# Kernel optimization log

Hardware: AMD Instinct MI355X
Metric: run time of the kernel (lower is better)

Reference implementation:

```python
import jax, jax.numpy as jnp
import numpy as np

B, S, H, A, I = 64, 512, 1024, 1024, 1024


def setup_inputs() -> dict:
    key = jax.random.key(0)
    ks = jax.random.split(key, 12)
    s = lambda fan_in: 1.0 / np.sqrt(fan_in)
    return {
        "encoded": jax.random.normal(ks[0], (B, S, H), jnp.float32),
        "inputs": jax.random.normal(ks[1], (B, I), jnp.float32),
        "states": jax.random.normal(ks[2], (B, H), jnp.float32),
        # attention params
        "W_enc": jax.random.uniform(ks[3], (H, A), jnp.float32, -s(H), s(H)),
        "b_enc": jnp.zeros((A,), jnp.float32),
        "W_dec": jax.random.uniform(ks[4], (H, A), jnp.float32, -s(H), s(H)),
        "b_dec": jnp.zeros((A,), jnp.float32),
        "w_out": jax.random.uniform(ks[5], (A, 1), jnp.float32, -s(A), s(A)),
        "b_out": jnp.zeros((1,), jnp.float32),
        # GRU cell params (input size = I + H)
        "W_ih": jax.random.uniform(ks[6], (3 * H, I + H), jnp.float32, -s(H), s(H)),
        "W_hh": jax.random.uniform(ks[7], (3 * H, H), jnp.float32, -s(H), s(H)),
        "b_ih": jax.random.uniform(ks[8], (3 * H,), jnp.float32, -s(H), s(H)),
        "b_hh": jax.random.uniform(ks[9], (3 * H,), jnp.float32, -s(H), s(H)),
    }


def reference(encoded, inputs, states, W_enc, b_enc, W_dec, b_dec, w_out, b_out,
              W_ih, W_hh, b_ih, b_hh):
    # setup_memory: project encoder states  [B,S,H] @ [H,A] -> [B,S,A]
    enc_proj = jnp.einsum("bsh,ha->bsa", encoded, W_enc) + b_enc
    # project decoder state and broadcast over S
    dec_proj = states @ W_dec + b_dec                      # [B,A]
    projected = enc_proj + dec_proj[:, None, :]            # [B,S,A]
    scores = jnp.tanh(projected) @ w_out + b_out           # [B,S,1]
    weights = jax.nn.softmax(scores, axis=1)               # [B,S,1]
    attention = jnp.sum(encoded * weights, axis=1)         # [B,H]
    # GRU cell on concatenated input
    x = jnp.concatenate([inputs, attention], axis=1)       # [B,I+H]
    gi = x @ W_ih.T + b_ih                                 # [B,3H]
    gh = states @ W_hh.T + b_hh                            # [B,3H]
    i_r, i_z, i_n = jnp.split(gi, 3, axis=1)
    h_r, h_z, h_n = jnp.split(gh, 3, axis=1)
    r = jax.nn.sigmoid(i_r + h_r)
    z = jax.nn.sigmoid(i_z + h_z)
    n = jnp.tanh(i_n + r * h_n)
    return (1.0 - z) * n + z * states                      # [B,H]
```

## Files before the change

kernel.cpp:

```cpp
#include <hip/hip_runtime.h>
#include <stdint.h>

typedef __bf16 bf16x8 __attribute__((ext_vector_type(8)));
typedef float f32x4 __attribute__((ext_vector_type(4)));

#define LOG2E 1.4426950408889634f
#define LSTR 32

__device__ __forceinline__ unsigned short f2bf(float f) {
  unsigned int x = __builtin_bit_cast(unsigned int, f);
  x += 0x7FFFu + ((x >> 16) & 1u);
  return (unsigned short)(x >> 16);
}
__device__ __forceinline__ float bflo(unsigned int u) {
  return __builtin_bit_cast(float, u << 16);
}
__device__ __forceinline__ float bfhi(unsigned int u) {
  return __builtin_bit_cast(float, u & 0xffff0000u);
}
__device__ __forceinline__ float tanh_fast(float x) {
  float cx = fminf(fmaxf(x, -15.f), 15.f);
  float e = __builtin_amdgcn_exp2f(cx * (2.f * LOG2E));
  return (e - 1.f) * __builtin_amdgcn_rcpf(e + 1.f);
}
__device__ __forceinline__ float sigmoid_fast(float x) {
  float cx = fminf(fmaxf(x, -30.f), 30.f);
  float e = __builtin_amdgcn_exp2f(cx * LOG2E);
  return e * __builtin_amdgcn_rcpf(e + 1.f);
}
__device__ __forceinline__ ushort4 cvt4(const float4 f) {
  return make_ushort4(f2bf(f.x), f2bf(f.y), f2bf(f.z), f2bf(f.w));
}

__device__ __forceinline__ void gl_lds16(const unsigned short* g,
                                         const unsigned short* lds_base) {
  __builtin_amdgcn_global_load_lds(
      (const __attribute__((address_space(1))) unsigned int*)(uintptr_t)g,
      (__attribute__((address_space(3))) unsigned int*)(unsigned int)(uintptr_t)lds_base,
      16, 0, 0);
}

__global__ __launch_bounds__(256) void k_prep(
    const float* __restrict__ W_enc, unsigned short* __restrict__ Wt,
    const float* __restrict__ states, const float* __restrict__ W_dec,
    const float* __restrict__ b_dec, const float* __restrict__ b_enc,
    float* __restrict__ dvec, float4* __restrict__ zbase,
    const float* __restrict__ enc, unsigned short* __restrict__ encb) {
  __shared__ unsigned short tile[64][65];
  __shared__ float red[256];
  const int bid = blockIdx.x;
  const int tid = threadIdx.x;
  if (bid < 256) {
    const int bx = bid & 15, by = bid >> 4;
    const int x = tid & 63, y0 = tid >> 6;
#pragma unroll
    for (int i = y0; i < 64; i += 4)
      tile[i][x] = f2bf(W_enc[(size_t)(by * 64 + i) * 1024 + bx * 64 + x]);
    __syncthreads();
#pragma unroll
    for (int i = y0; i < 64; i += 4)
      Wt[(size_t)(bx * 64 + i) * 1024 + by * 64 + x] = tile[x][i];
  } else if (bid < 768) {
    const int bb = bid - 256;
    const int b = bb >> 3;
    const int a0 = (bb & 7) * 128;
    const int a = tid & 127, half = tid >> 7;
    const float* sp = states + (size_t)b * 1024;
    const float* wp = W_dec + a0 + a;
    float acc = 0.f;
    const int kb = half * 512;
#pragma unroll 8
    for (int k = kb; k < kb + 512; ++k)
      acc += sp[k] * wp[(size_t)k * 1024];
    red[tid] = acc;
    __syncthreads();
    if (tid < 128) {
      float v = red[tid] + red[tid + 128];
      dvec[(size_t)b * 1024 + a0 + tid] = v + b_dec[a0 + tid] + b_enc[a0 + tid];
    }
  } else if (bid < 1248) {
    const float4 z = {0.f, 0.f, 0.f, 0.f};
    zbase[(size_t)(bid - 768) * 256 + tid] = z;
  } else {
    const size_t i = ((size_t)(bid - 1248) * 256 + tid) * 8;
    const float4 f0 = *(const float4*)(enc + i);
    const float4 f1 = *(const float4*)(enc + i + 4);
    *(ushort4*)(encb + i) = cvt4(f0);
    *(ushort4*)(encb + i + 4) = cvt4(f1);
  }
}

__global__ __launch_bounds__(256, 3) void k_scores_bf16(
    const unsigned short* __restrict__ encb,
    const unsigned short* __restrict__ Wt,
    const float* __restrict__ dvec,
    const float* __restrict__ w_out,
    float* __restrict__ scores) {
  __shared__ alignas(16) unsigned short lds[2][8192];
  __shared__ float sc[128];

  const int tid = threadIdx.x;
  const int wave = tid >> 6, lane = tid & 63;
  const int l15 = lane & 15, quad = lane >> 4;
  const int xcd = blockIdx.x & 7;
  const int kb_ = blockIdx.x >> 3;
  const int mt = ((kb_ >> 3) << 3) | xcd;
  const int nt = kb_ & 7;
  const int row0 = mt * 128;
  const int b = row0 >> 9;
  const int wm = (wave >> 1) * 64, wn = (wave & 1) * 64;
  const int srow = lane >> 2;
  const int fsw = ((lane >> 2) & 3) ^ ((lane >> 4) & 3);
  const int skoff = (((lane & 3) ^ fsw) * 8);
  const int rchunk = ((quad ^ ((l15 & 3) ^ ((l15 >> 2) & 3))) * 8);

  if (tid < 128) sc[tid] = 0.f;

  const unsigned short* gsrc[4];
#pragma unroll
  for (int s = 0; s < 4; ++s) {
    const int g = wave * 4 + s;
    gsrc[s] = (g < 8)
        ? encb + (size_t)(row0 + g * 16 + srow) * 1024 + skoff
        : Wt + (size_t)(nt * 128 + (g - 8) * 16 + srow) * 1024 + skoff;
  }

  const f32x4 vz = {0.f, 0.f, 0.f, 0.f};
  f32x4 acc[4][4];
#pragma unroll
  for (int i = 0; i < 4; ++i)
#pragma unroll
    for (int j = 0; j < 4; ++j) acc[i][j] = vz;

#define STAGE(BUF, KK)                                              \
  do {                                                              \
    _Pragma("unroll") for (int s = 0; s < 4; ++s)                   \
        gl_lds16(gsrc[s] + (KK), &lds[BUF][(wave * 4 + s) * 512]);  \
  } while (0)

#define COMPUTE(BUF)                                                          \
  do {                                                                        \
    bf16x8 af[4], bg[4];                                                      \
    _Pragma("unroll") for (int i = 0; i < 4; ++i)                             \
        af[i] = *(const bf16x8*)(&lds[BUF][(wm + i * 16 + l15) * LSTR + rchunk]); \
    _Pragma("unroll") for (int j = 0; j < 4; ++j)                             \
        bg[j] = *(const bf16x8*)(&lds[BUF][4096 + (wn + j * 16 + l15) * LSTR + rchunk]); \
    _Pragma("unroll") for (int i = 0; i < 4; ++i)                             \
      _Pragma("unroll") for (int j = 0; j < 4; ++j)                           \
          acc[i][j] = __builtin_amdgcn_mfma_f32_16x16x32_bf16(af[i], bg[j],   \
                                                              acc[i][j], 0, 0, 0); \
  } while (0)

  STAGE(0, 0);
  __syncthreads();

#pragma unroll 1
  for (int k0 = 0; k0 < 1024; k0 += 64) {
    STAGE(1, k0 + 32);
    COMPUTE(0);
    __syncthreads();
    if (k0 + 64 < 1024) { STAGE(0, k0 + 64); }
    COMPUTE(1);
    __syncthreads();
  }
#undef STAGE
#undef COMPUTE

  float p[4][4];
#pragma unroll
  for (int i = 0; i < 4; ++i)
#pragma unroll
    for (int r = 0; r < 4; ++r) p[i][r] = 0.f;
#pragma unroll
  for (int j = 0; j < 4; ++j) {
    const int a = nt * 128 + wn + j * 16 + l15;
    const float dv = dvec[(size_t)b * 1024 + a];
    const float wo = w_out[a];
#pragma unroll
    for (int i = 0; i < 4; ++i)
#pragma unroll
      for (int r = 0; r < 4; ++r)
        p[i][r] += tanh_fast(acc[i][j][r] + dv) * wo;
  }
#pragma unroll
  for (int i = 0; i < 4; ++i)
#pragma unroll
    for (int r = 0; r < 4; ++r) {
      float v = p[i][r];
      v += __shfl_xor(v, 1);
      v += __shfl_xor(v, 2);
      v += __shfl_xor(v, 4);
      v += __shfl_xor(v, 8);
      if (l15 == 0) atomicAdd(&sc[wm + i * 16 + quad * 4 + r], v);
    }
  __syncthreads();
  if (tid < 128)
    atomicAdd(&scores[(size_t)b * 512 + (row0 & 511) + tid], sc[tid]);
}

__global__ __launch_bounds__(256) void k_scores_f32(
    const float* __restrict__ enc, const unsigned short* __restrict__ Wt,
    const float* __restrict__ dvec, const float* __restrict__ w_out,
    float* __restrict__ scores) {
  __shared__ alignas(16) unsigned short lA[128 * LSTR];
  __shared__ alignas(16) unsigned short lB[128 * LSTR];
  __shared__ float sc[128];
  const int tid = threadIdx.x;
  const int wave = tid >> 6, lane = tid & 63;
  const int l15 = lane & 15, quad = lane >> 4;
  const int mt = blockIdx.x >> 2, nh = blockIdx.x & 3;
  const int row0 = mt * 128, b = row0 >> 9;
  const int wm = (wave >> 1) * 64, wn = (wave & 1) * 64;
  const int srow = lane >> 2, skoff = (lane & 3) * 8;
  if (tid < 128) sc[tid] = 0.f;
  const f32x4 vz = {0.f, 0.f, 0.f, 0.f};
#pragma unroll 1
  for (int t2 = 0; t2 < 2; ++t2) {
    const int nt = nh * 2 + t2;
    f32x4 acc[4][4];
#pragma unroll
    for (int i = 0; i < 4; ++i)
#pragma unroll
      for (int j = 0; j < 4; ++j) acc[i][j] = vz;
#pragma unroll 1
    for (int k0 = 0; k0 < 1024; k0 += 32) {
      ushort4 sa[2][2];
      uint4 vb[2];
#pragma unroll
      for (int rr = 0; rr < 2; ++rr) {
        const int r = wave * 2 + rr;
        const float* ap = enc + (size_t)(row0 + r * 16 + srow) * 1024 + k0 + skoff;
        sa[rr][0] = cvt4(*(const float4*)ap);
        sa[rr][1] = cvt4(*(const float4*)(ap + 4));
        vb[rr] = *(const uint4*)(Wt + (size_t)(nt * 128 + r * 16 + srow) * 1024 + k0 + skoff);
      }
      __syncthreads();
#pragma unroll
      for (int rr = 0; rr < 2; ++rr) {
        const int r = wave * 2 + rr;
        *(ushort4*)(lA + (r * 16 + srow) * LSTR + skoff) = sa[rr][0];
        *(ushort4*)(lA + (r * 16 + srow) * LSTR + skoff + 4) = sa[rr][1];
        *(uint4*)(lB + (r * 16 + srow) * LSTR + skoff) = vb[rr];
      }
      __syncthreads();
      bf16x8 af[4], bg[4];
#pragma unroll
      for (int i = 0; i < 4; ++i)
        af[i] = *(const bf16x8*)(lA + (wm + i * 16 + l15) * LSTR + quad * 8);
#pragma unroll
      for (int j = 0; j < 4; ++j)
        bg[j] = *(const bf16x8*)(lB + (wn + j * 16 + l15) * LSTR + quad * 8);
#pragma unroll
      for (int i = 0; i < 4; ++i)
#pragma unroll
        for (int j = 0; j < 4; ++j)
          acc[i][j] = __builtin_amdgcn_mfma_f32_16x16x32_bf16(af[i], bg[j],
                                                              acc[i][j], 0, 0, 0);
    }
    float p[4][4];
#pragma unroll
    for (int i = 0; i < 4; ++i)
#pragma unroll
      for (int r = 0; r < 4; ++r) p[i][r] = 0.f;
#pragma unroll
    for (int j = 0; j < 4; ++j) {
      const int a = nt * 128 + wn + j * 16 + l15;
      const float dv = dvec[(size_t)b * 1024 + a];
      const float wo = w_out[a];
#pragma unroll
      for (int i = 0; i < 4; ++i)
#pragma unroll
        for (int r = 0; r < 4; ++r)
          p[i][r] += tanh_fast(acc[i][j][r] + dv) * wo;
    }
#pragma unroll
    for (int i = 0; i < 4; ++i)
#pragma unroll
      for (int r = 0; r < 4; ++r) {
        float v = p[i][r];
        v += __shfl_xor(v, 1);
        v += __shfl_xor(v, 2);
        v += __shfl_xor(v, 4);
        v += __shfl_xor(v, 8);
        if (l15 == 0) atomicAdd(&sc[wm + i * 16 + quad * 4 + r], v);
      }
  }
  __syncthreads();
  if (tid < 128)
    atomicAdd(&scores[(size_t)b * 512 + (row0 & 511) + tid], sc[tid]);
}

template <bool ABF16>
__global__ __launch_bounds__(256) void k_attn(const void* __restrict__ encv,
                                              const float* __restrict__ scores,
                                              float* __restrict__ att) {
  const int b = blockIdx.x >> 2;
  const int scn = blockIdx.x & 3;
  const int tid = threadIdx.x;
  __shared__ float w[512];
  __shared__ float redm[4], reds[4];

  const float s0 = scores[(size_t)b * 512 + tid];
  const float s1 = scores[(size_t)b * 512 + 256 + tid];
  float m = fmaxf(s0, s1);
#pragma unroll
  for (int off = 32; off; off >>= 1) m = fmaxf(m, __shfl_xor(m, off));
  const int wv = tid >> 6;
  if ((tid & 63) == 0) redm[wv] = m;
  __syncthreads();
  m = fmaxf(fmaxf(redm[0], redm[1]), fmaxf(redm[2], redm[3]));
  const float e0 = __builtin_amdgcn_exp2f((s0 - m) * LOG2E);
  const float e1 = __builtin_amdgcn_exp2f((s1 - m) * LOG2E);
  float sum = e0 + e1;
#pragma unroll
  for (int off = 32; off; off >>= 1) sum += __shfl_xor(sum, off);
  if ((tid & 63) == 0) reds[wv] = sum;
  __syncthreads();
  sum = reds[0] + reds[1] + reds[2] + reds[3];
  const float inv = 1.f / sum;
  w[tid] = e0 * inv;
  w[tid + 256] = e1 * inv;
  __syncthreads();

  const int h0 = (tid & 127) * 8;
  const int sh = tid >> 7;
  float a[8];
#pragma unroll
  for (int i = 0; i < 8; ++i) a[i] = 0.f;
  const size_t base = ((size_t)(b * 512 + scn * 128 + sh)) * 1024 + h0;
#pragma unroll 4
  for (int i = 0; i < 64; ++i) {
    const float ws_ = w[scn * 128 + sh + 2 * i];
    if constexpr (ABF16) {
      const uint4 v = *(const uint4*)((const unsigned short*)encv + base + (size_t)(2 * i) * 1024);
      a[0] += ws_ * bflo(v.x); a[1] += ws_ * bfhi(v.x);
      a[2] += ws_ * bflo(v.y); a[3] += ws_ * bfhi(v.y);
      a[4] += ws_ * bflo(v.z); a[5] += ws_ * bfhi(v.z);
      a[6] += ws_ * bflo(v.w); a[7] += ws_ * bfhi(v.w);
    } else {
      const float* ep = (const float*)encv + base + (size_t)(2 * i) * 1024;
      const float4 v0 = *(const float4*)ep;
      const float4 v1 = *(const float4*)(ep + 4);
      a[0] += ws_ * v0.x; a[1] += ws_ * v0.y;
      a[2] += ws_ * v0.z; a[3] += ws_ * v0.w;
      a[4] += ws_ * v1.x; a[5] += ws_ * v1.y;
      a[6] += ws_ * v1.z; a[7] += ws_ * v1.w;
    }
  }
#pragma unroll
  for (int i = 0; i < 8; ++i)
    atomicAdd(&att[(size_t)b * 1024 + h0 + i], a[i]);
}

__global__ __launch_bounds__(256) void k_gru_gemm(
    const float* __restrict__ xin,
    const float* __restrict__ att,
    const float* __restrict__ states,
    const float* __restrict__ W_ih,
    const float* __restrict__ W_hh,
    float* __restrict__ gbuf) {
  const int tid = threadIdx.x;
  const int wave = tid >> 6, lane = tid & 63;
  const int l15 = lane & 15, quad = lane >> 4;
  const int kk = blockIdx.x & 3;
  const int rest = blockIdx.x >> 2;
  const bool is_gh = rest >= 48;
  const int nt = is_gh ? rest - 48 : rest;
  const int n0 = nt * 64;
  const int KT = is_gh ? 1024 : 2048;
  const int Kh = KT >> 2;
  const int kbase = kk * Kh;
  const float* W = is_gh ? W_hh : W_ih;
  float* outp = gbuf + (is_gh ? (size_t)64 * 3072 : 0);

  __shared__ alignas(16) unsigned short lA[64 * LSTR];
  __shared__ alignas(16) unsigned short lB[64 * LSTR];

  const f32x4 vz = {0.f, 0.f, 0.f, 0.f};
  f32x4 acc[2][2];
  acc[0][0] = vz; acc[0][1] = vz; acc[1][0] = vz; acc[1][1] = vz;

  const int arow = tid >> 2;
  const int achunk = (tid & 3) * 8;
  const int fswG = ((tid >> 2) & 3) ^ ((tid >> 4) & 3);
  const int wchunk = (((tid & 3) ^ fswG) * 8);
  const int rchunkG = ((quad ^ ((l15 & 3) ^ ((l15 >> 2) & 3))) * 8);
  const int wm2 = (wave >> 1) * 32, wn2 = (wave & 1) * 32;

  float4 ra0, ra1, rb0, rb1;
  auto LOADK = [&](int kg0) {
    const int kg = kg0 + achunk;
    const float* ap = is_gh ? (states + (size_t)arow * 1024 + kg)
                    : (kg < 1024 ? (xin + (size_t)arow * 1024 + kg)
                                 : (att + (size_t)arow * 1024 + (kg - 1024)));
    ra0 = *(const float4*)ap;
    ra1 = *(const float4*)(ap + 4);
    const float* wp = W + (size_t)(n0 + arow) * KT + kg;
    rb0 = *(const float4*)wp;
    rb1 = *(const float4*)(wp + 4);
  };
  LOADK(kbase);

#pragma unroll 1
  for (int k0 = 0; k0 < Kh; k0 += 32) {
    __syncthreads();
    *(ushort4*)(lA + arow * LSTR + wchunk) = cvt4(ra0);
    *(ushort4*)(lA + arow * LSTR + wchunk + 4) = cvt4(ra1);
    *(ushort4*)(lB + arow * LSTR + wchunk) = cvt4(rb0);
    *(ushort4*)(lB + arow * LSTR + wchunk + 4) = cvt4(rb1);
    __syncthreads();
    if (k0 + 32 < Kh) LOADK(kbase + k0 + 32);
    bf16x8 af[2], bg[2];
#pragma unroll
    for (int i = 0; i < 2; ++i)
      af[i] = *(const bf16x8*)(lA + (wm2 + i * 16 + l15) * LSTR + rchunkG);
#pragma unroll
    for (int j = 0; j < 2; ++j)
      bg[j] = *(const bf16x8*)(lB + (wn2 + j * 16 + l15) * LSTR + rchunkG);
#pragma unroll
    for (int i = 0; i < 2; ++i)
#pragma unroll
      for (int j = 0; j < 2; ++j)
        acc[i][j] = __builtin_amdgcn_mfma_f32_16x16x32_bf16(af[i], bg[j],
                                                            acc[i][j], 0, 0, 0);
  }
#pragma unroll
  for (int i = 0; i < 2; ++i)
#pragma unroll
    for (int j = 0; j < 2; ++j)
#pragma unroll
      for (int r = 0; r < 4; ++r) {
        const int m = wm2 + i * 16 + quad * 4 + r;
        const int n = n0 + wn2 + j * 16 + l15;
        atomicAdd(&outp[(size_t)m * 3072 + n], acc[i][j][r]);
      }
}

__global__ void k_gate(const float* __restrict__ gbuf,
                       const float* __restrict__ states,
                       const float* __restrict__ b_ih,
                       const float* __restrict__ b_hh,
                       float* __restrict__ outp) {
  const int idx = blockIdx.x * 256 + threadIdx.x;
  const int b = idx >> 10, h = idx & 1023;
  const float* gi = gbuf + (size_t)b * 3072;
  const float* gh = gbuf + (size_t)64 * 3072 + (size_t)b * 3072;
  const float ir = gi[h] + b_ih[h];
  const float iz = gi[1024 + h] + b_ih[1024 + h];
  const float in_ = gi[2048 + h] + b_ih[2048 + h];
  const float hr = gh[h] + b_hh[h];
  const float hz = gh[1024 + h] + b_hh[1024 + h];
  const float hn = gh[2048 + h] + b_hh[2048 + h];
  const float r = sigmoid_fast(ir + hr);
  const float z = sigmoid_fast(iz + hz);
  const float n = tanh_fast(in_ + r * hn);
  const float hp = states[idx];
  outp[idx] = (1.f - z) * n + z * hp;
}

extern "C" void kernel_launch(void* const* d_in, const int* in_sizes, int n_in,
                              void* d_out, int out_size, void* d_ws, size_t ws_size,
                              hipStream_t stream) {
  const float* enc    = (const float*)d_in[0];
  const float* xin    = (const float*)d_in[1];
  const float* states = (const float*)d_in[2];
  const float* W_enc  = (const float*)d_in[3];
  const float* b_enc  = (const float*)d_in[4];
  const float* W_dec  = (const float*)d_in[5];
  const float* b_dec  = (const float*)d_in[6];
  const float* w_out  = (const float*)d_in[7];
  const float* W_ih   = (const float*)d_in[9];
  const float* W_hh   = (const float*)d_in[10];
  const float* b_ih   = (const float*)d_in[11];
  const float* b_hh   = (const float*)d_in[12];
  float* out = (float*)d_out;

  const size_t ENC_BF16_BYTES = (size_t)32768 * 1024 * 2;
  const bool use_bf16 = ws_size >= ENC_BF16_BYTES + (8u << 20);

  char* ws = (char*)d_ws;
  unsigned short* encb = (unsigned short*)ws;
  char* base = ws + (use_bf16 ? ENC_BF16_BYTES : 0);
  unsigned short* Wt = (unsigned short*)base;
  float* dvec    = (float*)(base + 2097152);
  float* scoresb = (float*)(base + 2097152 + 262144);
  float* att     = (float*)(base + 2097152 + 262144 + 131072);
  float* gbuf    = (float*)(base + 2097152 + 262144 + 131072 + 262144);

  const int prep_grid = use_bf16 ? 17632 : 1248;
  k_prep<<<prep_grid, 256, 0, stream>>>(W_enc, Wt, states, W_dec, b_dec, b_enc,
                                        dvec, (float4*)scoresb, enc, encb);
  if (use_bf16) {
    k_scores_bf16<<<2048, 256, 0, stream>>>(encb, Wt, dvec, w_out, scoresb);
    k_attn<true><<<256, 256, 0, stream>>>(encb, scoresb, att);
  } else {
    k_scores_f32<<<1024, 256, 0, stream>>>(enc, Wt, dvec, w_out, scoresb);
    k_attn<false><<<256, 256, 0, stream>>>(enc, scoresb, att);
  }
  k_gru_gemm<<<384, 256, 0, stream>>>(xin, att, states, W_ih, W_hh, gbuf);
  k_gate<<<256, 256, 0, stream>>>(gbuf, states, b_ih, b_hh, out);
}
```

Measured before the change: 405.5 us.

## Replace atomic accumulations in attention and GRU GEMM with deterministic reductions

The attention kernel now gives each block the full sequence for a 128-wide slice of H. It reduces partial sums across sequence groups in LDS and stores the result directly, so float atomics into att are gone. The GRU GEMM writes each split-K partial to its own plane of gbuf, and the gate kernel sums the four planes. With att and gbuf no longer accumulated through atomics, the prep kernel zeroes only the scores buffer, which cuts most of the zero-fill blocks. In exchange, the gate kernel reads more memory, the attention kernel adds LDS reduction barriers, and gbuf now reuses the start of the bf16 encoder workspace after that data is consumed.

```diff
diff --git a/kernel.cpp b/kernel.cpp
--- a/kernel.cpp
+++ b/kernel.cpp
@@ -78,11 +78,11 @@
       float v = red[tid] + red[tid + 128];
       dvec[(size_t)b * 1024 + a0 + tid] = v + b_dec[a0 + tid] + b_enc[a0 + tid];
     }
-  } else if (bid < 1248) {
+  } else if (bid < 800) {
     const float4 z = {0.f, 0.f, 0.f, 0.f};
     zbase[(size_t)(bid - 768) * 256 + tid] = z;
   } else {
-    const size_t i = ((size_t)(bid - 1248) * 256 + tid) * 8;
+    const size_t i = ((size_t)(bid - 800) * 256 + tid) * 8;
     const float4 f0 = *(const float4*)(enc + i);
     const float4 f1 = *(const float4*)(enc + i + 4);
     *(ushort4*)(encb + i) = cvt4(f0);
@@ -294,11 +294,12 @@
 __global__ __launch_bounds__(256) void k_attn(const void* __restrict__ encv,
                                               const float* __restrict__ scores,
                                               float* __restrict__ att) {
-  const int b = blockIdx.x >> 2;
-  const int scn = blockIdx.x & 3;
+  const int b = blockIdx.x >> 3;
+  const int hch = blockIdx.x & 7;
   const int tid = threadIdx.x;
   __shared__ float w[512];
   __shared__ float redm[4], reds[4];
+  __shared__ float red[16][132];
 
   const float s0 = scores[(size_t)b * 512 + tid];
   const float s1 = scores[(size_t)b * 512 + 256 + tid];
@@ -322,23 +323,25 @@
   w[tid + 256] = e1 * inv;
   __syncthreads();
 
-  const int h0 = (tid & 127) * 8;
-  const int sh = tid >> 7;
+  const int sgrp = tid >> 4;
+  const int hsub = tid & 15;
+  const int h0 = hch * 128 + hsub * 8;
   float a[8];
 #pragma unroll
-  for (int i = 0; i < 8; ++i) a[i] = 0.f;
-  const size_t base = ((size_t)(b * 512 + scn * 128 + sh)) * 1024 + h0;
-#pragma unroll 4
-  for (int i = 0; i < 64; ++i) {
-    const float ws_ = w[scn * 128 + sh + 2 * i];
+  for (int j = 0; j < 8; ++j) a[j] = 0.f;
+#pragma unroll 8
+  for (int si = 0; si < 32; ++si) {
+    const int s = si * 16 + sgrp;
+    const float ws_ = w[s];
     if constexpr (ABF16) {
-      const uint4 v = *(const uint4*)((const unsigned short*)encv + base + (size_t)(2 * i) * 1024);
+      const uint4 v = *(const uint4*)((const unsigned short*)encv +
+                                      (size_t)(b * 512 + s) * 1024 + h0);
       a[0] += ws_ * bflo(v.x); a[1] += ws_ * bfhi(v.x);
       a[2] += ws_ * bflo(v.y); a[3] += ws_ * bfhi(v.y);
       a[4] += ws_ * bflo(v.z); a[5] += ws_ * bfhi(v.z);
       a[6] += ws_ * bflo(v.w); a[7] += ws_ * bfhi(v.w);
     } else {
-      const float* ep = (const float*)encv + base + (size_t)(2 * i) * 1024;
+      const float* ep = (const float*)encv + (size_t)(b * 512 + s) * 1024 + h0;
       const float4 v0 = *(const float4*)ep;
       const float4 v1 = *(const float4*)(ep + 4);
       a[0] += ws_ * v0.x; a[1] += ws_ * v0.y;
@@ -348,8 +351,25 @@
     }
   }
 #pragma unroll
-  for (int i = 0; i < 8; ++i)
-    atomicAdd(&att[(size_t)b * 1024 + h0 + i], a[i]);
+  for (int j = 0; j < 8; ++j) red[sgrp][hsub * 8 + j] = a[j];
+  __syncthreads();
+#pragma unroll
+  for (int step = 8; step >= 1; step >>= 1) {
+    if (sgrp < step) {
+#pragma unroll
+      for (int j = 0; j < 8; ++j)
+        red[sgrp][hsub * 8 + j] += red[sgrp + step][hsub * 8 + j];
+    }
+    __syncthreads();
+  }
+  if (sgrp == 0) {
+    float4 o0 = {red[0][hsub * 8 + 0], red[0][hsub * 8 + 1],
+                 red[0][hsub * 8 + 2], red[0][hsub * 8 + 3]};
+    float4 o1 = {red[0][hsub * 8 + 4], red[0][hsub * 8 + 5],
+                 red[0][hsub * 8 + 6], red[0][hsub * 8 + 7]};
+    *(float4*)(att + (size_t)b * 1024 + h0) = o0;
+    *(float4*)(att + (size_t)b * 1024 + h0 + 4) = o1;
+  }
 }
 
 __global__ __launch_bounds__(256) void k_gru_gemm(
@@ -371,7 +391,8 @@
   const int Kh = KT >> 2;
   const int kbase = kk * Kh;
   const float* W = is_gh ? W_hh : W_ih;
-  float* outp = gbuf + (is_gh ? (size_t)64 * 3072 : 0);
+  const int plane = is_gh ? 4 + kk : kk;
+  float* outp = gbuf + (size_t)plane * 64 * 3072;
 
   __shared__ alignas(16) unsigned short lA[64 * LSTR];
   __shared__ alignas(16) unsigned short lB[64 * LSTR];
@@ -432,7 +453,7 @@
       for (int r = 0; r < 4; ++r) {
         const int m = wm2 + i * 16 + quad * 4 + r;
         const int n = n0 + wn2 + j * 16 + l15;
-        atomicAdd(&outp[(size_t)m * 3072 + n], acc[i][j][r]);
+        outp[(size_t)m * 3072 + n] = acc[i][j][r];
       }
 }
 
@@ -443,14 +464,20 @@
                        float* __restrict__ outp) {
   const int idx = blockIdx.x * 256 + threadIdx.x;
   const int b = idx >> 10, h = idx & 1023;
-  const float* gi = gbuf + (size_t)b * 3072;
-  const float* gh = gbuf + (size_t)64 * 3072 + (size_t)b * 3072;
-  const float ir = gi[h] + b_ih[h];
-  const float iz = gi[1024 + h] + b_ih[1024 + h];
-  const float in_ = gi[2048 + h] + b_ih[2048 + h];
-  const float hr = gh[h] + b_hh[h];
-  const float hz = gh[1024 + h] + b_hh[1024 + h];
-  const float hn = gh[2048 + h] + b_hh[2048 + h];
+  float gir = 0.f, giz = 0.f, gin = 0.f, ghr = 0.f, ghz = 0.f, ghn = 0.f;
+#pragma unroll
+  for (int p = 0; p < 4; ++p) {
+    const float* gi = gbuf + ((size_t)p * 64 + b) * 3072;
+    gir += gi[h]; giz += gi[1024 + h]; gin += gi[2048 + h];
+    const float* gh = gbuf + ((size_t)(4 + p) * 64 + b) * 3072;
+    ghr += gh[h]; ghz += gh[1024 + h]; ghn += gh[2048 + h];
+  }
+  const float ir = gir + b_ih[h];
+  const float iz = giz + b_ih[1024 + h];
+  const float in_ = gin + b_ih[2048 + h];
+  const float hr = ghr + b_hh[h];
+  const float hz = ghz + b_hh[1024 + h];
+  const float hn = ghn + b_hh[2048 + h];
   const float r = sigmoid_fast(ir + hr);
   const float z = sigmoid_fast(iz + hz);
   const float n = tanh_fast(in_ + r * hn);
@@ -485,17 +512,17 @@
   float* dvec    = (float*)(base + 2097152);
   float* scoresb = (float*)(base + 2097152 + 262144);
   float* att     = (float*)(base + 2097152 + 262144 + 131072);
-  float* gbuf    = (float*)(base + 2097152 + 262144 + 131072 + 262144);
-
-  const int prep_grid = use_bf16 ? 17632 : 1248;
+  float* gbuf = use_bf16 ? (float*)ws : (float*)(base + (4u << 20));
+
+  const int prep_grid = use_bf16 ? 17184 : 800;
   k_prep<<<prep_grid, 256, 0, stream>>>(W_enc, Wt, states, W_dec, b_dec, b_enc,
                                         dvec, (float4*)scoresb, enc, encb);
   if (use_bf16) {
     k_scores_bf16<<<2048, 256, 0, stream>>>(encb, Wt, dvec, w_out, scoresb);
-    k_attn<true><<<256, 256, 0, stream>>>(encb, scoresb, att);
+    k_attn<true><<<512, 256, 0, stream>>>(encb, scoresb, att);
   } else {
     k_scores_f32<<<1024, 256, 0, stream>>>(enc, Wt, dvec, w_out, scoresb);
-    k_attn<false><<<256, 256, 0, stream>>>(enc, scoresb, att);
+    k_attn<false><<<512, 256, 0, stream>>>(enc, scoresb, att);
   }
   k_gru_gemm<<<384, 256, 0, stream>>>(xin, att, states, W_ih, W_hh, gbuf);
   k_gate<<<256, 256, 0, stream>>>(gbuf, states, b_ih, b_hh, out);
```

Measured after the change: 395.5 us. 2.5% less time.
